# Kernel tuning notes

Hardware: AMD Instinct MI355X
Metric: run time of the kernel (lower is better)

Reference implementation:

```python
import jax, jax.numpy as jnp
import numpy as np

N = 65536   # number of input points
M = 4096    # subsample_size (centroids)
K = 64      # group_limit (neighborhood size)
RADIUS = 0.2  # group_radius


def _mlp(x, W1, b1, W2, b2, W3, b3):
    # PyG MLP([6, 64, 64, 128], act='relu'); batch_norm with default running
    # stats (mean 0, var 1) is identity, so: Linear-ReLU-Linear-ReLU-Linear.
    h = jax.nn.relu(x @ W1 + b1)
    h = jax.nn.relu(h @ W2 + b2)
    return h @ W3 + b3


def setup_inputs() -> dict:
    key = jax.random.key(0)
    ks = jax.random.split(key, 8)
    vertices = jax.random.normal(ks[0], (N, 3), dtype=jnp.float32)
    centroid_indices = jax.random.randint(ks[1], (M,), 0, N)

    def lin(k, fi, fo):
        return (jax.random.normal(k, (fi, fo), dtype=jnp.float32) / np.sqrt(fi)).astype(jnp.float32)

    return {
        "vertices": vertices,
        "centroid_indices": centroid_indices,
        "W1": lin(ks[2], 6, 64),  "b1": jnp.zeros((64,), jnp.float32),
        "W2": lin(ks[3], 64, 64), "b2": jnp.zeros((64,), jnp.float32),
        "W3": lin(ks[4], 64, 128), "b3": jnp.zeros((128,), jnp.float32),
    }


def reference(vertices, centroid_indices, W1, b1, W2, b2, W3, b3):
    # --- group_around_centroids ---
    sq_norm = jnp.einsum('ij,ij->i', vertices, vertices)          # [N]
    cpos = vertices[centroid_indices]                              # [M,3]
    # faithful distance formula: sqrt(|sn_c - 2 c.v + sn|)
    d = jnp.sqrt(jnp.abs(sq_norm[centroid_indices][:, None]
                         - 2.0 * (cpos @ vertices.T)
                         + sq_norm[None, :]))                      # [M,N]  (~1 GB)
    # K nearest per centroid (equivalent to masking by k-th sorted distance)
    neg_dk, idx = jax.lax.top_k(-d, K)                             # [M,K]
    d_k = -neg_dk                                                  # ascending distances
    limit = jnp.minimum(d_k[:, K - 1], RADIUS)                     # [M]
    mask = d_k <= limit[:, None]                                   # [M,K]

    # --- PointNetConv: msg = MLP(cat[x_j, pos_j - pos_i]), max-aggregate to centroid ---
    pos_j = vertices[idx]                                          # [M,K,3]
    feat = jnp.concatenate([pos_j, pos_j - cpos[:, None, :]], axis=-1)  # [M,K,6]
    h = _mlp(feat, W1, b1, W2, b2, W3, b3)                         # [M,K,128]
    h = jnp.where(mask[:, :, None], h, -jnp.inf)
    return jnp.max(h, axis=1)                                      # [M,128]
```

## Files before the change

kernel.cpp:

```cpp
#include <hip/hip_runtime.h>
#include <hip/hip_bf16.h>

#define GD     50
#define NC     (GD*GD*GD)
#define CAPK   256
#define RADIUS_F 0.2f
#define R2SAFE 0.0401f

typedef unsigned long long ull;
typedef __attribute__((ext_vector_type(4))) _Float16 f16x4;
typedef __attribute__((ext_vector_type(8))) _Float16 f16x8;
typedef __attribute__((ext_vector_type(4))) float    f32x4;

__device__ __forceinline__ int cellcoord(float v) {
    int c = (int)floorf((v + 5.0f) * 5.0f);
    return min(max(c, 0), GD - 1);
}

__global__ void sa_zero_kernel(int4* __restrict__ dst, int n4) {
    int i = blockIdx.x * blockDim.x + threadIdx.x;
    int stride = gridDim.x * blockDim.x;
    for (; i < n4; i += stride) dst[i] = make_int4(0, 0, 0, 0);
}

__global__ void sa_prep_kernel(const float* __restrict__ vtx,
                               float4* __restrict__ pt4,
                               int* __restrict__ cid,
                               int* __restrict__ cellCnt,
                               int N,
                               const float* __restrict__ W1,
                               const float* __restrict__ W2,
                               const float* __restrict__ W3,
                               _Float16* __restrict__ wf16) {
    int i = blockIdx.x * blockDim.x + threadIdx.x;
    int stride = gridDim.x * blockDim.x;
    for (int p = i; p < N; p += stride) {
        float x = vtx[3 * p], y = vtx[3 * p + 1], z = vtx[3 * p + 2];
        float sn = fmaf(z, z, fmaf(y, y, x * x));
        pt4[p] = make_float4(x, y, z, sn);
        int cc = (cellcoord(z) * GD + cellcoord(y)) * GD + cellcoord(x);
        cid[p] = cc;
        atomicAdd(&cellCnt[cc], 1);
    }
    for (int e = i; e < 1024; e += stride) {
        int col = e >> 4, k = e & 15;
        wf16[e] = (k < 6) ? (_Float16)W1[k * 64 + col] : (_Float16)0.f;
    }
    for (int e = i; e < 4096; e += stride) {
        int col = e >> 6, k = e & 63;
        wf16[1024 + e] = (_Float16)W2[k * 64 + col];
    }
    for (int e = i; e < 8192; e += stride) {
        int col = e >> 6, k = e & 63;
        wf16[5120 + e] = (_Float16)W3[k * 128 + col];
    }
}

__global__ __launch_bounds__(256) void sa_offsets_kernel(
    const int* __restrict__ cellCnt, int* __restrict__ cellStart,
    int* __restrict__ cellCur, int* __restrict__ cursor) {
    __shared__ int sc[256];
    __shared__ int base_s;
    int t = threadIdx.x;
    int i = blockIdx.x * 256 + t;
    int c = (i < NC) ? cellCnt[i] : 0;
    sc[t] = c;
    __syncthreads();
    for (int d = 1; d < 256; d <<= 1) {
        int o = (t >= d) ? sc[t - d] : 0;
        __syncthreads();
        sc[t] += o;
        __syncthreads();
    }
    if (t == 255) base_s = atomicAdd(cursor, sc[255]);
    __syncthreads();
    int start = base_s + sc[t] - c;
    if (i < NC) { cellStart[i] = start; cellCur[i] = start; }
}

__global__ void sa_scatter_kernel(const float4* __restrict__ pt4,
                                  const int* __restrict__ cid,
                                  int* __restrict__ cellCur,
                                  float4* __restrict__ sorted4,
                                  int* __restrict__ sidx, int N) {
    int p = blockIdx.x * blockDim.x + threadIdx.x;
    if (p < N) {
        int pos = atomicAdd(&cellCur[cid[p]], 1);
        sorted4[pos] = pt4[p];
        sidx[pos] = p;
    }
}

__global__ __launch_bounds__(256) void sa_fused2_kernel(
    const float4* __restrict__ pt4, const int* __restrict__ cidx,
    const float4* __restrict__ sorted4, const int* __restrict__ sidx,
    const int* __restrict__ cellCnt, const int* __restrict__ cellStart,
    const _Float16* __restrict__ wf16,
    const float* __restrict__ b1, const float* __restrict__ b2,
    const float* __restrict__ b3, float* __restrict__ out) {

    __shared__ __align__(16) char smem[4][8192];
    __shared__ int selb[4][64];
    __shared__ int scnt_s[4];

    int t = threadIdx.x, w = t >> 6, lane = t & 63;
    int c = blockIdx.x * 4 + w;
    float4 cc = pt4[cidx[c]];

    ull* key = (ull*)smem[w];
    _Float16* featb = (_Float16*)(smem[w] + 4096);
    _Float16* h = (_Float16*)smem[w];

    int cx = cellcoord(cc.x), cy = cellcoord(cc.y), cz = cellcoord(cc.z);
    int x0 = max(cx - 1, 0), x1 = min(cx + 1, GD - 1), lx = x1 - x0 + 1;
    int y0 = max(cy - 1, 0), y1 = min(cy + 1, GD - 1), ly = y1 - y0 + 1;
    int z0 = max(cz - 1, 0), z1 = min(cz + 1, GD - 1), lz = z1 - z0 + 1;
    int L = lx * ly * lz;

    int cellc = 0, cstart = 0;
    if (lane < L) {
        int lxy = lx * ly;
        int iz = lane / lxy, rem = lane - iz * lxy;
        int iy = rem / lx, ix = rem - iy * lx;
        int gx = x0 + ix, gy = y0 + iy, gz = z0 + iz;
        float xlo = (gx == 0) ? -1e30f : gx * 0.2f - 5.0f;
        float xhi = (gx == GD - 1) ? 1e30f : (gx + 1) * 0.2f - 5.0f;
        float ylo = (gy == 0) ? -1e30f : gy * 0.2f - 5.0f;
        float yhi = (gy == GD - 1) ? 1e30f : (gy + 1) * 0.2f - 5.0f;
        float zlo = (gz == 0) ? -1e30f : gz * 0.2f - 5.0f;
        float zhi = (gz == GD - 1) ? 1e30f : (gz + 1) * 0.2f - 5.0f;
        float dx = fmaxf(0.f, fmaxf(xlo - cc.x, cc.x - xhi));
        float dy = fmaxf(0.f, fmaxf(ylo - cc.y, cc.y - yhi));
        float dz = fmaxf(0.f, fmaxf(zlo - cc.z, cc.z - zhi));
        if (fmaf(dz, dz, fmaf(dy, dy, dx * dx)) <= R2SAFE) {
            int cell = (gz * GD + gy) * GD + gx;
            cellc = cellCnt[cell];
            cstart = cellStart[cell];
        }
    }
    int pfx = cellc;
#pragma unroll
    for (int d = 1; d < 32; d <<= 1) {
        int o = __shfl_up(pfx, d);
        if (lane >= d) pfx += o;
    }
    int excl = pfx - cellc;
    if (lane == 0) scnt_s[w] = 0;
    int T = __shfl(pfx, L - 1);

    for (int base = 0; base < T; base += 64) {
        int s = base + lane;
        int lo = 0, hi = L - 1;
#pragma unroll 5
        for (int it = 0; it < 5; ++it) {
            int mid = (lo + hi + 1) >> 1;
            int em = __shfl(excl, mid);
            if (lo < hi) { if (em <= s) lo = mid; else hi = mid - 1; }
        }
        int sp = __shfl(cstart, lo) + (s - __shfl(excl, lo));
        if (s < T) {
            float4 p = sorted4[sp];
            float dot = fmaf(p.z, cc.z, fmaf(p.y, cc.y, p.x * cc.x));
            float tt = fmaf(-2.f, dot, cc.w) + p.w;
            if (tt <= R2SAFE) {
                float d = sqrtf(fabsf(tt));
                if (d <= RADIUS_F) {
                    int pid = sidx[sp];
                    int slot = atomicAdd(&scnt_s[w], 1);
                    if (slot < CAPK)
                        key[slot] = (((ull)__float_as_uint(d)) << 32) | (unsigned)pid;
                }
            }
        }
    }

    int n = min(scnt_s[w], CAPK);
    int nsel = min(n, 64);
    if (n > 64) {
        for (int i = lane; i < n; i += 64) {
            ull ki = key[i];
            int r = 0;
            for (int j = 0; j < n; ++j) r += (key[j] < ki) ? 1 : 0;
            if (r < 64) selb[w][r] = (int)(unsigned)(ki & 0xffffffffu);
        }
    } else {
        for (int i = lane; i < n; i += 64)
            selb[w][i] = (int)(unsigned)(key[i] & 0xffffffffu);
    }

    {
        _Float16 z = (_Float16)0.f;
        f16x8 lo8 = {z, z, z, z, z, z, z, z};
        if (lane < nsel) {
            float4 p = pt4[selb[w][lane]];
            lo8[0] = (_Float16)p.x; lo8[1] = (_Float16)p.y; lo8[2] = (_Float16)p.z;
            lo8[3] = (_Float16)(p.x - cc.x);
            lo8[4] = (_Float16)(p.y - cc.y);
            lo8[5] = (_Float16)(p.z - cc.z);
        }
        f16x8 hi8 = {z, z, z, z, z, z, z, z};
        *(f16x8*)&featb[lane * 16 + 0] = lo8;
        *(f16x8*)&featb[lane * 16 + 8] = hi8;
    }

    int r16 = lane & 15, g = lane >> 4;
    const _Float16* w1 = wf16;
    const _Float16* w2 = wf16 + 1024;
    const _Float16* w3 = wf16 + 5120;

    {
        f16x4 a1[4];
#pragma unroll
        for (int m = 0; m < 4; ++m)
            a1[m] = *(const f16x4*)&featb[(m * 16 + r16) * 16 + g * 4];
#pragma unroll
        for (int nn = 0; nn < 4; ++nn) {
            int col = nn * 16 + r16;
            f16x4 b = *(const f16x4*)&w1[col * 16 + g * 4];
            float bb = b1[col];
#pragma unroll
            for (int m = 0; m < 4; ++m) {
                f32x4 acc = {bb, bb, bb, bb};
                acc = __builtin_amdgcn_mfma_f32_16x16x16f16(a1[m], b, acc, 0, 0, 0);
#pragma unroll
                for (int reg = 0; reg < 4; ++reg) {
                    int row = m * 16 + g * 4 + reg;
                    h[row * 64 + (col ^ ((row & 7) << 3))] =
                        (_Float16)fmaxf(acc[reg], 0.f);
                }
            }
        }
    }

    {
        f16x8 a2[4][2];
#pragma unroll
        for (int m = 0; m < 4; ++m)
#pragma unroll
            for (int kt = 0; kt < 2; ++kt) {
                int row = m * 16 + r16;
                int k0 = kt * 32 + g * 8;
                a2[m][kt] = *(const f16x8*)&h[row * 64 + (k0 ^ ((row & 7) << 3))];
            }
#pragma unroll
        for (int nn = 0; nn < 4; ++nn) {
            int col = nn * 16 + r16;
            f16x8 bA = *(const f16x8*)&w2[col * 64 + g * 8];
            f16x8 bB = *(const f16x8*)&w2[col * 64 + 32 + g * 8];
            float bb = b2[col];
#pragma unroll
            for (int m = 0; m < 4; ++m) {
                f32x4 acc = {bb, bb, bb, bb};
                acc = __builtin_amdgcn_mfma_f32_16x16x32_f16(a2[m][0], bA, acc, 0, 0, 0);
                acc = __builtin_amdgcn_mfma_f32_16x16x32_f16(a2[m][1], bB, acc, 0, 0, 0);
#pragma unroll
                for (int reg = 0; reg < 4; ++reg) {
                    int row = m * 16 + g * 4 + reg;
                    h[row * 64 + (col ^ ((row & 7) << 3))] =
                        (_Float16)fmaxf(acc[reg], 0.f);
                }
            }
        }
    }

    {
        f16x8 a3[4][2];
#pragma unroll
        for (int m = 0; m < 4; ++m)
#pragma unroll
            for (int kt = 0; kt < 2; ++kt) {
                int row = m * 16 + r16;
                int k0 = kt * 32 + g * 8;
                a3[m][kt] = *(const f16x8*)&h[row * 64 + (k0 ^ ((row & 7) << 3))];
            }
        float ninf = __int_as_float(0xff800000);
#pragma unroll
        for (int nn = 0; nn < 8; ++nn) {
            int col = nn * 16 + r16;
            f16x8 bA = *(const f16x8*)&w3[col * 64 + g * 8];
            f16x8 bB = *(const f16x8*)&w3[col * 64 + 32 + g * 8];
            float bb = b3[col];
            float vm = ninf;
#pragma unroll
            for (int m = 0; m < 4; ++m) {
                f32x4 acc = {bb, bb, bb, bb};
                acc = __builtin_amdgcn_mfma_f32_16x16x32_f16(a3[m][0], bA, acc, 0, 0, 0);
                acc = __builtin_amdgcn_mfma_f32_16x16x32_f16(a3[m][1], bB, acc, 0, 0, 0);
#pragma unroll
                for (int reg = 0; reg < 4; ++reg) {
                    int row = m * 16 + g * 4 + reg;
                    if (row < nsel) vm = fmaxf(vm, acc[reg]);
                }
            }
            vm = fmaxf(vm, __shfl_xor(vm, 16));
            vm = fmaxf(vm, __shfl_xor(vm, 32));
            if (lane < 16) out[(size_t)c * 128 + nn * 16 + lane] = vm;
        }
    }
}

extern "C" void kernel_launch(void* const* d_in, const int* in_sizes, int n_in,
                              void* d_out, int out_size, void* d_ws, size_t ws_size,
                              hipStream_t stream) {
    const float* vtx = (const float*)d_in[0];
    const int* cidx  = (const int*)d_in[1];
    const float* W1  = (const float*)d_in[2];
    const float* b1  = (const float*)d_in[3];
    const float* W2  = (const float*)d_in[4];
    const float* b2  = (const float*)d_in[5];
    const float* W3  = (const float*)d_in[6];
    const float* b3  = (const float*)d_in[7];
    float* out = (float*)d_out;

    int N = in_sizes[0] / 3;
    int M = in_sizes[1];

    char* ws = (char*)d_ws;
    size_t off = 0;
    float4* pt4     = (float4*)(ws + off); off += (size_t)N * 16;
    float4* sorted4 = (float4*)(ws + off); off += (size_t)N * 16;
    int* sidx       = (int*)(ws + off);    off += (size_t)N * 4;
    int* cid        = (int*)(ws + off);    off += (size_t)N * 4;
    int* cellCnt    = (int*)(ws + off);    off += (size_t)NC * 4;
    int* cursor     = (int*)(ws + off);    off += 16;
    int* cellStart  = (int*)(ws + off);    off += (size_t)NC * 4;
    int* cellCur    = (int*)(ws + off);    off += (size_t)NC * 4;
    _Float16* wf16  = (_Float16*)(ws + off);

    sa_zero_kernel<<<256, 256, 0, stream>>>((int4*)cellCnt, (NC * 4 + 16) / 16);
    sa_prep_kernel<<<512, 256, 0, stream>>>(vtx, pt4, cid, cellCnt, N,
                                            W1, W2, W3, wf16);
    sa_offsets_kernel<<<(NC + 255) / 256, 256, 0, stream>>>(cellCnt, cellStart,
                                                            cellCur, cursor);
    sa_scatter_kernel<<<(N + 255) / 256, 256, 0, stream>>>(pt4, cid, cellCur,
                                                           sorted4, sidx, N);
    sa_fused2_kernel<<<M / 4, 256, 0, stream>>>(pt4, cidx, sorted4, sidx,
                                                cellCnt, cellStart, wf16,
                                                b1, b2, b3, out);
}
```

Baseline: 72.85 us.

## Make x-rows contiguous in cell grid and scan neighbor rows directly

The offsets kernel now scans each z-slice serially inside one block, so all cells in a slice are laid out contiguously and an x-run of three neighbouring cells becomes one contiguous range. The fused kernel then iterates over up to 9 (y,z) rows with a direct index, which replaces the per-element binary search over 27 cells and drops the x-side cell culling. The fused kernel also changes from 4 waves per block to one wave per block. The trade-offs are that a few extra points from culled x-cells get tested, the offsets kernel runs fewer, longer blocks, and many tiny blocks are launched.

```diff
diff --git a/kernel.cpp b/kernel.cpp
--- a/kernel.cpp
+++ b/kernel.cpp
@@ -3,6 +3,7 @@
 
 #define GD     50
 #define NC     (GD*GD*GD)
+#define SLICE  (GD*GD)
 #define CAPK   256
 #define RADIUS_F 0.2f
 #define R2SAFE 0.0401f
@@ -60,22 +61,32 @@
     const int* __restrict__ cellCnt, int* __restrict__ cellStart,
     int* __restrict__ cellCur, int* __restrict__ cursor) {
     __shared__ int sc[256];
-    __shared__ int base_s;
+    __shared__ int sbase;
     int t = threadIdx.x;
-    int i = blockIdx.x * 256 + t;
-    int c = (i < NC) ? cellCnt[i] : 0;
-    sc[t] = c;
+    int base0 = blockIdx.x * SLICE;
+    int run = 0;
+    for (int chunk = 0; chunk < (SLICE + 255) / 256; ++chunk) {
+        int li = chunk * 256 + t;
+        int c = (li < SLICE) ? cellCnt[base0 + li] : 0;
+        sc[t] = c;
+        __syncthreads();
+        for (int d = 1; d < 256; d <<= 1) {
+            int o = (t >= d) ? sc[t - d] : 0;
+            __syncthreads();
+            sc[t] += o;
+            __syncthreads();
+        }
+        if (li < SLICE) cellStart[base0 + li] = run + sc[t] - c;
+        run += sc[255];
+        __syncthreads();
+    }
+    if (t == 0) sbase = atomicAdd(cursor, run);
     __syncthreads();
-    for (int d = 1; d < 256; d <<= 1) {
-        int o = (t >= d) ? sc[t - d] : 0;
-        __syncthreads();
-        sc[t] += o;
-        __syncthreads();
-    }
-    if (t == 255) base_s = atomicAdd(cursor, sc[255]);
-    __syncthreads();
-    int start = base_s + sc[t] - c;
-    if (i < NC) { cellStart[i] = start; cellCur[i] = start; }
+    for (int li = t; li < SLICE; li += 256) {
+        int s = cellStart[base0 + li] + sbase;
+        cellStart[base0 + li] = s;
+        cellCur[base0 + li] = s;
+    }
 }
 
 __global__ void sa_scatter_kernel(const float4* __restrict__ pt4,
@@ -91,7 +102,7 @@
     }
 }
 
-__global__ __launch_bounds__(256) void sa_fused2_kernel(
+__global__ __launch_bounds__(64) void sa_fused2_kernel(
     const float4* __restrict__ pt4, const int* __restrict__ cidx,
     const float4* __restrict__ sorted4, const int* __restrict__ sidx,
     const int* __restrict__ cellCnt, const int* __restrict__ cellStart,
@@ -99,100 +110,86 @@
     const float* __restrict__ b1, const float* __restrict__ b2,
     const float* __restrict__ b3, float* __restrict__ out) {
 
-    __shared__ __align__(16) char smem[4][8192];
-    __shared__ int selb[4][64];
-    __shared__ int scnt_s[4];
-
-    int t = threadIdx.x, w = t >> 6, lane = t & 63;
-    int c = blockIdx.x * 4 + w;
+    __shared__ __align__(16) char smem[8192];
+    __shared__ int selb[64];
+    __shared__ int scnt_s;
+
+    int lane = threadIdx.x;
+    int c = blockIdx.x;
     float4 cc = pt4[cidx[c]];
 
-    ull* key = (ull*)smem[w];
-    _Float16* featb = (_Float16*)(smem[w] + 4096);
-    _Float16* h = (_Float16*)smem[w];
+    ull* key = (ull*)smem;
+    _Float16* featb = (_Float16*)(smem + 4096);
+    _Float16* h = (_Float16*)smem;
 
     int cx = cellcoord(cc.x), cy = cellcoord(cc.y), cz = cellcoord(cc.z);
     int x0 = max(cx - 1, 0), x1 = min(cx + 1, GD - 1), lx = x1 - x0 + 1;
     int y0 = max(cy - 1, 0), y1 = min(cy + 1, GD - 1), ly = y1 - y0 + 1;
     int z0 = max(cz - 1, 0), z1 = min(cz + 1, GD - 1), lz = z1 - z0 + 1;
-    int L = lx * ly * lz;
-
-    int cellc = 0, cstart = 0;
-    if (lane < L) {
-        int lxy = lx * ly;
-        int iz = lane / lxy, rem = lane - iz * lxy;
-        int iy = rem / lx, ix = rem - iy * lx;
-        int gx = x0 + ix, gy = y0 + iy, gz = z0 + iz;
-        float xlo = (gx == 0) ? -1e30f : gx * 0.2f - 5.0f;
-        float xhi = (gx == GD - 1) ? 1e30f : (gx + 1) * 0.2f - 5.0f;
+    int nrow = ly * lz;
+
+    int rstart = 0, rlen = 0;
+    if (lane < nrow) {
+        int iy = lane % ly, iz = lane / ly;
+        int gy = y0 + iy, gz = z0 + iz;
         float ylo = (gy == 0) ? -1e30f : gy * 0.2f - 5.0f;
         float yhi = (gy == GD - 1) ? 1e30f : (gy + 1) * 0.2f - 5.0f;
         float zlo = (gz == 0) ? -1e30f : gz * 0.2f - 5.0f;
         float zhi = (gz == GD - 1) ? 1e30f : (gz + 1) * 0.2f - 5.0f;
-        float dx = fmaxf(0.f, fmaxf(xlo - cc.x, cc.x - xhi));
         float dy = fmaxf(0.f, fmaxf(ylo - cc.y, cc.y - yhi));
         float dz = fmaxf(0.f, fmaxf(zlo - cc.z, cc.z - zhi));
-        if (fmaf(dz, dz, fmaf(dy, dy, dx * dx)) <= R2SAFE) {
-            int cell = (gz * GD + gy) * GD + gx;
-            cellc = cellCnt[cell];
-            cstart = cellStart[cell];
-        }
-    }
-    int pfx = cellc;
-#pragma unroll
-    for (int d = 1; d < 32; d <<= 1) {
-        int o = __shfl_up(pfx, d);
-        if (lane >= d) pfx += o;
-    }
-    int excl = pfx - cellc;
-    if (lane == 0) scnt_s[w] = 0;
-    int T = __shfl(pfx, L - 1);
-
-    for (int base = 0; base < T; base += 64) {
-        int s = base + lane;
-        int lo = 0, hi = L - 1;
-#pragma unroll 5
-        for (int it = 0; it < 5; ++it) {
-            int mid = (lo + hi + 1) >> 1;
-            int em = __shfl(excl, mid);
-            if (lo < hi) { if (em <= s) lo = mid; else hi = mid - 1; }
-        }
-        int sp = __shfl(cstart, lo) + (s - __shfl(excl, lo));
-        if (s < T) {
-            float4 p = sorted4[sp];
-            float dot = fmaf(p.z, cc.z, fmaf(p.y, cc.y, p.x * cc.x));
-            float tt = fmaf(-2.f, dot, cc.w) + p.w;
-            if (tt <= R2SAFE) {
-                float d = sqrtf(fabsf(tt));
-                if (d <= RADIUS_F) {
-                    int pid = sidx[sp];
-                    int slot = atomicAdd(&scnt_s[w], 1);
-                    if (slot < CAPK)
-                        key[slot] = (((ull)__float_as_uint(d)) << 32) | (unsigned)pid;
+        if (fmaf(dz, dz, dy * dy) <= R2SAFE) {
+            int cell0 = (gz * GD + gy) * GD + x0;
+            int cellL = cell0 + (lx - 1);
+            rstart = cellStart[cell0];
+            rlen = cellStart[cellL] + cellCnt[cellL] - rstart;
+        }
+    }
+    if (lane == 0) scnt_s = 0;
+
+    for (int r = 0; r < nrow; ++r) {
+        int len = __shfl(rlen, r);
+        if (len == 0) continue;
+        int st = __shfl(rstart, r);
+        for (int b = 0; b < len; b += 64) {
+            int i = b + lane;
+            if (i < len) {
+                int sp = st + i;
+                float4 p = sorted4[sp];
+                float dot = fmaf(p.z, cc.z, fmaf(p.y, cc.y, p.x * cc.x));
+                float tt = fmaf(-2.f, dot, cc.w) + p.w;
+                if (tt <= R2SAFE) {
+                    float d = sqrtf(fabsf(tt));
+                    if (d <= RADIUS_F) {
+                        int pid = sidx[sp];
+                        int slot = atomicAdd(&scnt_s, 1);
+                        if (slot < CAPK)
+                            key[slot] = (((ull)__float_as_uint(d)) << 32) | (unsigned)pid;
+                    }
                 }
             }
         }
     }
 
-    int n = min(scnt_s[w], CAPK);
+    int n = min(scnt_s, CAPK);
     int nsel = min(n, 64);
     if (n > 64) {
         for (int i = lane; i < n; i += 64) {
             ull ki = key[i];
             int r = 0;
             for (int j = 0; j < n; ++j) r += (key[j] < ki) ? 1 : 0;
-            if (r < 64) selb[w][r] = (int)(unsigned)(ki & 0xffffffffu);
+            if (r < 64) selb[r] = (int)(unsigned)(ki & 0xffffffffu);
         }
     } else {
         for (int i = lane; i < n; i += 64)
-            selb[w][i] = (int)(unsigned)(key[i] & 0xffffffffu);
+            selb[i] = (int)(unsigned)(key[i] & 0xffffffffu);
     }
 
     {
         _Float16 z = (_Float16)0.f;
         f16x8 lo8 = {z, z, z, z, z, z, z, z};
         if (lane < nsel) {
-            float4 p = pt4[selb[w][lane]];
+            float4 p = pt4[selb[lane]];
             lo8[0] = (_Float16)p.x; lo8[1] = (_Float16)p.y; lo8[2] = (_Float16)p.z;
             lo8[3] = (_Float16)(p.x - cc.x);
             lo8[4] = (_Float16)(p.y - cc.y);
@@ -330,11 +327,11 @@
     sa_zero_kernel<<<256, 256, 0, stream>>>((int4*)cellCnt, (NC * 4 + 16) / 16);
     sa_prep_kernel<<<512, 256, 0, stream>>>(vtx, pt4, cid, cellCnt, N,
                                             W1, W2, W3, wf16);
-    sa_offsets_kernel<<<(NC + 255) / 256, 256, 0, stream>>>(cellCnt, cellStart,
-                                                            cellCur, cursor);
+    sa_offsets_kernel<<<GD, 256, 0, stream>>>(cellCnt, cellStart,
+                                              cellCur, cursor);
     sa_scatter_kernel<<<(N + 255) / 256, 256, 0, stream>>>(pt4, cid, cellCur,
                                                            sorted4, sidx, N);
-    sa_fused2_kernel<<<M / 4, 256, 0, stream>>>(pt4, cidx, sorted4, sidx,
-                                                cellCnt, cellStart, wf16,
-                                                b1, b2, b3, out);
-}
+    sa_fused2_kernel<<<M, 64, 0, stream>>>(pt4, cidx, sorted4, sidx,
+                                           cellCnt, cellStart, wf16,
+                                           b1, b2, b3, out);
+}
```

Result: slower. 84.70 us (+16.3%).
